# Kernel optimization log

Measured on AMD Instinct MI355X. Metric: run time of the kernel, lower is better.

## Reference

```python
import jax, jax.numpy as jnp
from jax import lax
import numpy as np

INPUT_SIZE = 4
HIDDEN = 64
PROJ = 52


def setup_inputs() -> dict:
    key = jax.random.key(0)
    ks = jax.random.split(key, 6)
    k = 1.0 / np.sqrt(HIDDEN)  # PyTorch LSTM init range
    u = lambda kk, shape: jax.random.uniform(kk, shape, jnp.float32, -k, k)
    return {
        "x": jax.random.normal(ks[0], (4096, 512, INPUT_SIZE), jnp.float32),
        "W_ih": u(ks[1], (4 * HIDDEN, INPUT_SIZE)),   # gates [i,f,g,o]
        "W_hh": u(ks[2], (4 * HIDDEN, PROJ)),          # recurrent acts on projected h
        "b_ih": u(ks[3], (4 * HIDDEN,)),
        "b_hh": u(ks[4], (4 * HIDDEN,)),
        "W_hr": u(ks[5], (PROJ, HIDDEN)),              # projection h = W_hr @ (o*tanh(c))
    }


def reference(x, W_ih, W_hh, b_ih, b_hh, W_hr):
    B = x.shape[0]
    b = b_ih + b_hh
    xT = jnp.swapaxes(x, 0, 1)  # [T, B, input]

    def step(carry, xt):
        h, c = carry  # h: [B, PROJ], c: [B, HIDDEN]
        gates = xt @ W_ih.T + h @ W_hh.T + b  # [B, 4H]
        i, f, g, o = jnp.split(gates, 4, axis=-1)
        i = jax.nn.sigmoid(i)
        f = jax.nn.sigmoid(f)
        g = jnp.tanh(g)
        o = jax.nn.sigmoid(o)
        c = f * c + i * g
        h = (o * jnp.tanh(c)) @ W_hr.T  # projected hidden state
        return (h, c), None

    h0 = jnp.zeros((B, PROJ), x.dtype)
    c0 = jnp.zeros((B, HIDDEN), x.dtype)
    (h_last, _), _ = lax.scan(step, (h0, c0), xT)
    return h_last  # [B, PROJ] == r_out[:, -1, :]
```

## Files before the change

### kernel.cpp

```cpp
#include <hip/hip_runtime.h>


#define T_STEPS 512
#define HID 64
#define NPROJ 52
#define NBATCH 16
#define ROWB 136
#define DBYTES (NBATCH * ROWB)
#define XBYTES (T_STEPS * 128)
#define LOG2E 1.44269504088896340736f

typedef _Float16 half8 __attribute__((ext_vector_type(8)));
typedef float f32x4 __attribute__((ext_vector_type(4)));

__device__ __forceinline__ float exp2_f(float x) {
#if __has_builtin(__builtin_amdgcn_exp2f)
    return __builtin_amdgcn_exp2f(x);
#else
    return exp2f(x);
#endif
}
__device__ __forceinline__ float rcp_f(float x) {
    return __builtin_amdgcn_rcpf(x);
}

__global__ __launch_bounds__(256, 1)
void lstmp_kernel(const float* __restrict__ x,
                  const float* __restrict__ Wih,
                  const float* __restrict__ Whh,
                  const float* __restrict__ bih,
                  const float* __restrict__ bhh,
                  const float* __restrict__ Whr,
                  float* __restrict__ out)
{
    __shared__ char lds[XBYTES + 2 * DBYTES];
    char* xl = lds;
    char* dl = lds + XBYTES;

    const int lane = threadIdx.x & 63;
    const int wave = threadIdx.x >> 6;
    const int quad = lane >> 4;
    const int col  = lane & 15;

    {
        unsigned* p = (unsigned*)dl;
        for (int i = threadIdx.x; i < (int)(2 * DBYTES / 4); i += 256) p[i] = 0u;
    }

    {
        const float4* xg = (const float4*)x + (size_t)blockIdx.x * NBATCH * T_STEPS;
        for (int i = threadIdx.x; i < NBATCH * T_STEPS; i += 256) {
            const int b = i >> 9;
            const int t = i & (T_STEPS - 1);
            const float4 v = xg[i];
            union { _Float16 h[4]; unsigned long long q; } u;
            u.h[0] = (_Float16)v.x; u.h[1] = (_Float16)v.y;
            u.h[2] = (_Float16)v.z; u.h[3] = (_Float16)v.w;
            *(unsigned long long*)(xl + t * 128 + b * 8) = u.q;
        }
    }

    const int hid = wave * 16 + col;
    float macc[4][16];
#pragma unroll
    for (int g = 0; g < 4; ++g)
#pragma unroll
        for (int kk = 0; kk < 16; ++kk) macc[g][kk] = 0.0f;

    for (int p = 0; p < NPROJ; ++p) {
        float wv[4];
#pragma unroll
        for (int g = 0; g < 4; ++g) wv[g] = Whh[(g * HID + hid) * NPROJ + p];
        const float* wr = Whr + p * HID + quad * 8;
        const float4 r0 = *(const float4*)(wr);
        const float4 r1 = *(const float4*)(wr + 4);
        const float4 r2 = *(const float4*)(wr + 32);
        const float4 r3 = *(const float4*)(wr + 36);
        const float rk[16] = {r0.x, r0.y, r0.z, r0.w, r1.x, r1.y, r1.z, r1.w,
                              r2.x, r2.y, r2.z, r2.w, r3.x, r3.y, r3.z, r3.w};
#pragma unroll
        for (int g = 0; g < 4; ++g)
#pragma unroll
            for (int kk = 0; kk < 16; ++kk) macc[g][kk] = fmaf(wv[g], rk[kk], macc[g][kk]);
    }

    half8 aM[4][2];
    half8 aXB[4];
#pragma unroll
    for (int g = 0; g < 4; ++g) {
        const float scale = (g == 2) ? (2.0f * LOG2E) : LOG2E;
#pragma unroll
        for (int ch = 0; ch < 2; ++ch)
#pragma unroll
            for (int j = 0; j < 8; ++j)
                aM[g][ch][j] = (_Float16)(macc[g][ch * 8 + j] * scale);
        const int row = g * HID + hid;
#pragma unroll
        for (int j = 0; j < 8; ++j) {
            const int k = quad * 8 + j;
            float v = 0.0f;
            if (k < 4)       v = Wih[row * 4 + k];
            else if (k == 4) v = bih[row] + bhh[row];
            aXB[g][j] = (_Float16)(v * scale);
        }
    }

    float cacc[4] = {0.0f, 0.0f, 0.0f, 0.0f};

    const int dwoff  = col * ROWB + wave * 32 + quad * 8;
    const int drbase = col * ROWB + quad * 16;
    const char* xrd  = xl + col * 8;

    __syncthreads();

#pragma unroll 1
    for (int t = 0; t < T_STEPS; ++t) {
        const char* rbuf = dl + (t & 1) * DBYTES;
        char* wbuf = dl + ((t + 1) & 1) * DBYTES;

        half8 bd0, bd1;
        {
            const char* p0 = rbuf + drbase;
            union { unsigned long long q[2]; half8 h; } u0, u1;
            u0.q[0] = *(const unsigned long long*)(p0);
            u0.q[1] = *(const unsigned long long*)(p0 + 8);
            u1.q[0] = *(const unsigned long long*)(p0 + 64);
            u1.q[1] = *(const unsigned long long*)(p0 + 72);
            bd0 = u0.h; bd1 = u1.h;
        }
        half8 bx;
#pragma unroll
        for (int j = 0; j < 8; ++j) bx[j] = (_Float16)0.0f;
        if (quad == 0) {
            union { unsigned long long q; _Float16 h[4]; } u;
            u.q = *(const unsigned long long*)(xrd + t * 128);
            bx[0] = u.h[0]; bx[1] = u.h[1]; bx[2] = u.h[2]; bx[3] = u.h[3];
            bx[4] = (_Float16)1.0f;
        }

        const f32x4 z = {0.f, 0.f, 0.f, 0.f};
        f32x4 ai, af_, ag_, ao_;
        ai  = __builtin_amdgcn_mfma_f32_16x16x32_f16(aXB[0], bx, z, 0, 0, 0);
        af_ = __builtin_amdgcn_mfma_f32_16x16x32_f16(aXB[1], bx, z, 0, 0, 0);
        ag_ = __builtin_amdgcn_mfma_f32_16x16x32_f16(aXB[2], bx, z, 0, 0, 0);
        ao_ = __builtin_amdgcn_mfma_f32_16x16x32_f16(aXB[3], bx, ao_ = z, 0, 0, 0);
        ai  = __builtin_amdgcn_mfma_f32_16x16x32_f16(aM[0][0], bd0, ai,  0, 0, 0);
        af_ = __builtin_amdgcn_mfma_f32_16x16x32_f16(aM[1][0], bd0, af_, 0, 0, 0);
        ag_ = __builtin_amdgcn_mfma_f32_16x16x32_f16(aM[2][0], bd0, ag_, 0, 0, 0);
        ao_ = __builtin_amdgcn_mfma_f32_16x16x32_f16(aM[3][0], bd0, ao_, 0, 0, 0);
        ai  = __builtin_amdgcn_mfma_f32_16x16x32_f16(aM[0][1], bd1, ai,  0, 0, 0);
        af_ = __builtin_amdgcn_mfma_f32_16x16x32_f16(aM[1][1], bd1, af_, 0, 0, 0);
        ag_ = __builtin_amdgcn_mfma_f32_16x16x32_f16(aM[2][1], bd1, ag_, 0, 0, 0);
        ao_ = __builtin_amdgcn_mfma_f32_16x16x32_f16(aM[3][1], bd1, ao_, 0, 0, 0);

        union { _Float16 h[4]; unsigned long long q; } du;
#pragma unroll
        for (int r = 0; r < 4; ++r) {
            const float iv = rcp_f(1.0f + exp2_f(-ai[r]));
            const float fv = rcp_f(1.0f + exp2_f(-af_[r]));
            const float ov = rcp_f(1.0f + exp2_f(-ao_[r]));
            const float gs = fmaf(-4.0f * LOG2E, rcp_f(1.0f + exp2_f(ag_[r])),
                                  2.0f * LOG2E);
            const float cn = fmaf(fv, cacc[r], iv * gs);
            cacc[r] = cn;
            const float th = fmaf(-2.0f, rcp_f(1.0f + exp2_f(cn)), 1.0f);
            du.h[r] = (_Float16)(ov * th);
        }
        *(unsigned long long*)(wbuf + dwoff) = du.q;

        __syncthreads();
    }

    half8 aP[2];
    const int prow = wave * 16 + col;
#pragma unroll
    for (int ch = 0; ch < 2; ++ch)
#pragma unroll
        for (int j = 0; j < 8; ++j) {
            const int k = ch * 32 + quad * 8 + j;
            aP[ch][j] = (_Float16)((prow < NPROJ) ? Whr[prow * HID + k] : 0.0f);
        }

    half8 bd0, bd1;
    {
        const char* p0 = dl + 0 * DBYTES + drbase;
        union { unsigned long long q[2]; half8 h; } u0, u1;
        u0.q[0] = *(const unsigned long long*)(p0);
        u0.q[1] = *(const unsigned long long*)(p0 + 8);
        u1.q[0] = *(const unsigned long long*)(p0 + 64);
        u1.q[1] = *(const unsigned long long*)(p0 + 72);
        bd0 = u0.h; bd1 = u1.h;
    }
    f32x4 hf = {0.f, 0.f, 0.f, 0.f};
    hf = __builtin_amdgcn_mfma_f32_16x16x32_f16(aP[0], bd0, hf, 0, 0, 0);
    hf = __builtin_amdgcn_mfma_f32_16x16x32_f16(aP[1], bd1, hf, 0, 0, 0);

    const size_t bg = (size_t)blockIdx.x * NBATCH + col;
    float* o = out + bg * NPROJ;
    const int p0 = wave * 16 + quad * 4;
#pragma unroll
    for (int r = 0; r < 4; ++r) {
        const int p = p0 + r;
        if (p < NPROJ) o[p] = hf[r];
    }
}

extern "C" void kernel_launch(void* const* d_in, const int* in_sizes, int n_in,
                              void* d_out, int out_size, void* d_ws, size_t ws_size,
                              hipStream_t stream) {
    const float* x   = (const float*)d_in[0];
    const float* Wih = (const float*)d_in[1];
    const float* Whh = (const float*)d_in[2];
    const float* bih = (const float*)d_in[3];
    const float* bhh = (const float*)d_in[4];
    const float* Whr = (const float*)d_in[5];
    float* out = (float*)d_out;

    dim3 grid(4096 / NBATCH);
    dim3 block(256);
    lstmp_kernel<<<grid, block, 0, stream>>>(x, Wih, Whh, bih, bhh, Whr, out);
}
```

Before: 314.6 us.

## Split batch tile into two independent groups and interleave MFMA with activations

The 16-batch tile is split into two groups of 8 with their own recurrent state buffers. Each half-step runs the transcendental activation/cell update for one group while issuing the gate MFMAs for the other. The goal is to hide the serial MFMA-to-activation latency of the recurrence through cross-group ILP. In exchange, each lane does half the activation work per stage, but MFMA count and barrier count per time step both double, since the 16-wide MFMA now carries duplicated columns.

```diff
diff --git a/kernel.cpp b/kernel.cpp
--- a/kernel.cpp
+++ b/kernel.cpp
@@ -6,7 +6,7 @@
 #define NPROJ 52
 #define NBATCH 16
 #define ROWB 136
-#define DBYTES (NBATCH * ROWB)
+#define DGB (8 * ROWB)
 #define XBYTES (T_STEPS * 128)
 #define LOG2E 1.44269504088896340736f
 
@@ -33,18 +33,21 @@
                   const float* __restrict__ Whr,
                   float* __restrict__ out)
 {
-    __shared__ char lds[XBYTES + 2 * DBYTES];
+    __shared__ char lds[XBYTES + 2 * DGB];
     char* xl = lds;
-    char* dl = lds + XBYTES;
+    char* dA = lds + XBYTES;
+    char* dB = dA + DGB;
 
     const int lane = threadIdx.x & 63;
     const int wave = threadIdx.x >> 6;
     const int quad = lane >> 4;
     const int col  = lane & 15;
+    const bool low = col < 8;
+    const int bloc = col & 7;
 
     {
-        unsigned* p = (unsigned*)dl;
-        for (int i = threadIdx.x; i < (int)(2 * DBYTES / 4); i += 256) p[i] = 0u;
+        unsigned* p = (unsigned*)dA;
+        for (int i = threadIdx.x; i < (int)(2 * DGB / 4); i += 256) p[i] = 0u;
     }
 
     {
@@ -105,22 +108,20 @@
         }
     }
 
-    float cacc[4] = {0.0f, 0.0f, 0.0f, 0.0f};
-
-    const int dwoff  = col * ROWB + wave * 32 + quad * 8;
-    const int drbase = col * ROWB + quad * 16;
-    const char* xrd  = xl + col * 8;
+    float cA[2] = {0.0f, 0.0f}, cB[2] = {0.0f, 0.0f};
+    f32x4 pA[4], pB[4];
+
+    const int drbase = bloc * ROWB + quad * 16;
+    const int dwoff  = bloc * ROWB + (16 * wave + quad * 4 + (low ? 0 : 2)) * 2;
+    const char* xrdA = xl + bloc * 8;
+    const char* xrdB = xl + (bloc + 8) * 8;
 
     __syncthreads();
 
-#pragma unroll 1
-    for (int t = 0; t < T_STEPS; ++t) {
-        const char* rbuf = dl + (t & 1) * DBYTES;
-        char* wbuf = dl + ((t + 1) & 1) * DBYTES;
-
+    auto mfma_gates = [&](const char* dbuf, const char* xcell, f32x4* pr) {
         half8 bd0, bd1;
         {
-            const char* p0 = rbuf + drbase;
+            const char* p0 = dbuf + drbase;
             union { unsigned long long q[2]; half8 h; } u0, u1;
             u0.q[0] = *(const unsigned long long*)(p0);
             u0.q[1] = *(const unsigned long long*)(p0 + 8);
@@ -133,17 +134,16 @@
         for (int j = 0; j < 8; ++j) bx[j] = (_Float16)0.0f;
         if (quad == 0) {
             union { unsigned long long q; _Float16 h[4]; } u;
-            u.q = *(const unsigned long long*)(xrd + t * 128);
+            u.q = *(const unsigned long long*)xcell;
             bx[0] = u.h[0]; bx[1] = u.h[1]; bx[2] = u.h[2]; bx[3] = u.h[3];
             bx[4] = (_Float16)1.0f;
         }
-
         const f32x4 z = {0.f, 0.f, 0.f, 0.f};
         f32x4 ai, af_, ag_, ao_;
         ai  = __builtin_amdgcn_mfma_f32_16x16x32_f16(aXB[0], bx, z, 0, 0, 0);
         af_ = __builtin_amdgcn_mfma_f32_16x16x32_f16(aXB[1], bx, z, 0, 0, 0);
         ag_ = __builtin_amdgcn_mfma_f32_16x16x32_f16(aXB[2], bx, z, 0, 0, 0);
-        ao_ = __builtin_amdgcn_mfma_f32_16x16x32_f16(aXB[3], bx, ao_ = z, 0, 0, 0);
+        ao_ = __builtin_amdgcn_mfma_f32_16x16x32_f16(aXB[3], bx, z, 0, 0, 0);
         ai  = __builtin_amdgcn_mfma_f32_16x16x32_f16(aM[0][0], bd0, ai,  0, 0, 0);
         af_ = __builtin_amdgcn_mfma_f32_16x16x32_f16(aM[1][0], bd0, af_, 0, 0, 0);
         ag_ = __builtin_amdgcn_mfma_f32_16x16x32_f16(aM[2][0], bd0, ag_, 0, 0, 0);
@@ -152,22 +152,40 @@
         af_ = __builtin_amdgcn_mfma_f32_16x16x32_f16(aM[1][1], bd1, af_, 0, 0, 0);
         ag_ = __builtin_amdgcn_mfma_f32_16x16x32_f16(aM[2][1], bd1, ag_, 0, 0, 0);
         ao_ = __builtin_amdgcn_mfma_f32_16x16x32_f16(aM[3][1], bd1, ao_, 0, 0, 0);
-
-        union { _Float16 h[4]; unsigned long long q; } du;
-#pragma unroll
-        for (int r = 0; r < 4; ++r) {
-            const float iv = rcp_f(1.0f + exp2_f(-ai[r]));
-            const float fv = rcp_f(1.0f + exp2_f(-af_[r]));
-            const float ov = rcp_f(1.0f + exp2_f(-ao_[r]));
-            const float gs = fmaf(-4.0f * LOG2E, rcp_f(1.0f + exp2_f(ag_[r])),
+        pr[0] = ai; pr[1] = af_; pr[2] = ag_; pr[3] = ao_;
+    };
+
+    auto act_stage = [&](const f32x4* pr, float* cc, char* wbuf) {
+        union { _Float16 h[2]; unsigned w; } du;
+#pragma unroll
+        for (int u = 0; u < 2; ++u) {
+            const int rsel = (low ? 0 : 2) + u;
+            const float yi = pr[0][rsel], yf = pr[1][rsel];
+            const float yg = pr[2][rsel], yo = pr[3][rsel];
+            const float iv = rcp_f(1.0f + exp2_f(-yi));
+            const float fv = rcp_f(1.0f + exp2_f(-yf));
+            const float ov = rcp_f(1.0f + exp2_f(-yo));
+            const float gs = fmaf(-4.0f * LOG2E, rcp_f(1.0f + exp2_f(yg)),
                                   2.0f * LOG2E);
-            const float cn = fmaf(fv, cacc[r], iv * gs);
-            cacc[r] = cn;
+            const float cn = fmaf(fv, cc[u], iv * gs);
+            cc[u] = cn;
             const float th = fmaf(-2.0f, rcp_f(1.0f + exp2_f(cn)), 1.0f);
-            du.h[r] = (_Float16)(ov * th);
-        }
-        *(unsigned long long*)(wbuf + dwoff) = du.q;
-
+            du.h[u] = (_Float16)(ov * th);
+        }
+        *(unsigned*)(wbuf + dwoff) = du.w;
+    };
+
+    mfma_gates(dA, xrdA + 0 * 128, pA);
+
+#pragma unroll 1
+    for (int t = 0; t < T_STEPS; ++t) {
+        act_stage(pA, cA, dA);
+        mfma_gates(dB, xrdB + t * 128, pB);
+        __syncthreads();
+
+        act_stage(pB, cB, dB);
+        const int tn = (t + 1 < T_STEPS) ? (t + 1) : (T_STEPS - 1);
+        mfma_gates(dA, xrdA + tn * 128, pA);
         __syncthreads();
     }
 
@@ -183,7 +201,7 @@
 
     half8 bd0, bd1;
     {
-        const char* p0 = dl + 0 * DBYTES + drbase;
+        const char* p0 = (low ? dA : dB) + drbase;
         union { unsigned long long q[2]; half8 h; } u0, u1;
         u0.q[0] = *(const unsigned long long*)(p0);
         u0.q[1] = *(const unsigned long long*)(p0 + 8);
```

After: 463.3 us. 47.3% more time.
